# Kernel optimization log

Hardware: AMD Instinct MI355X
Metric: run time of the kernel (lower is better)

Reference implementation:

```python
import jax, jax.numpy as jnp
import numpy as np

DIM = 1024
NUM_HEADS = 16
HEAD_DIM = DIM // NUM_HEADS
ROPE_BASE = 10000.0


def _rope_cos_sin(seq_len, head_dim):
    inv_freq = 1.0 / (ROPE_BASE ** (jnp.arange(0, head_dim, 2, dtype=jnp.float32) / head_dim))
    t = jnp.arange(seq_len, dtype=jnp.float32)
    freqs = t[:, None] * inv_freq[None, :]            # [S, Dh/2]
    emb = jnp.concatenate([freqs, freqs], axis=-1)    # [S, Dh]
    return jnp.cos(emb), jnp.sin(emb)


def _rotate_half(x):
    half = x.shape[-1] // 2
    return jnp.concatenate([-x[..., half:], x[..., :half]], axis=-1)


def setup_inputs() -> dict:
    key = jax.random.key(0)
    k1, k2, k3 = jax.random.split(key, 3)
    B, S = 2, 2048
    x = jax.random.normal(k1, (B, S, DIM), dtype=jnp.float32)
    w_qkv = jax.random.normal(k2, (3 * DIM, DIM), dtype=jnp.float32) * (DIM ** -0.5)
    w_out = jax.random.normal(k3, (DIM, DIM), dtype=jnp.float32) * (DIM ** -0.5)
    return {"x": x, "w_qkv": w_qkv, "w_out": w_out}


def reference(x, w_qkv, w_out):
    B, S, D = x.shape
    H, Dh = NUM_HEADS, HEAD_DIM
    scale = Dh ** -0.5

    qkv = (x @ w_qkv.T).reshape(B, S, 3, H, Dh)      # [B,S,3,H,Dh]
    qkv = jnp.transpose(qkv, (2, 0, 3, 1, 4))        # [3,B,H,S,Dh]
    q, k, v = qkv[0], qkv[1], qkv[2]

    cos, sin = _rope_cos_sin(S, Dh)                  # [S,Dh]
    cos = cos[None, None, :, :]
    sin = sin[None, None, :, :]
    q = q * cos + _rotate_half(q) * sin
    k = k * cos + _rotate_half(k) * sin

    scores = jnp.einsum('bhqd,bhkd->bhqk', q, k) * scale
    causal_mask = jnp.triu(jnp.ones((S, S), dtype=bool), k=1)
    scores = jnp.where(causal_mask[None, None], -jnp.inf, scores)
    attn = jax.nn.softmax(scores, axis=-1)
    out = jnp.einsum('bhqk,bhkd->bhqd', attn, v)      # [B,H,S,Dh]
    out = jnp.transpose(out, (0, 2, 1, 3)).reshape(B, S, D)
    return out @ w_out.T
```

## Files before the change

### kernel.cpp

```cpp
#include <hip/hip_runtime.h>
#include <stdint.h>

typedef uint16_t u16;
typedef __attribute__((ext_vector_type(8))) short bf16x8;
typedef __attribute__((ext_vector_type(4))) float f32x4;

__device__ inline u16 f2b(float f) {
  uint32_t u = __float_as_uint(f);
  u += 0x7FFF + ((u >> 16) & 1);
  return (u16)(u >> 16);
}
__device__ inline float b2f(u16 h) {
  return __uint_as_float(((uint32_t)h) << 16);
}

typedef __attribute__((address_space(1))) void gvoid;
typedef __attribute__((address_space(3))) void lvoid;
#define GLOAD16(gp, lp)                                                        \
  __builtin_amdgcn_global_load_lds((gvoid*)(gp), (lvoid*)(lp), 16, 0, 0)

__global__ void k_detect(const u16* __restrict__ X, int* __restrict__ flag) {
  __shared__ int cnt;
  const int t = threadIdx.x;
  if (t == 0) cnt = 0;
  __syncthreads();
  float av = fabsf(b2f(X[t * 2]));
  int wild = (av < 1000.0f) ? 0 : 1;
  atomicAdd(&cnt, wild);
  __syncthreads();
  if (t == 0) flag[0] = (cnt > 16) ? 1 : 0;
}

__global__ __launch_bounds__(256, 4) void k_qkv_rope(const void* __restrict__ Xv,
                                                     const void* __restrict__ Wv,
                                                     const int* __restrict__ flag,
                                                     u16* __restrict__ Qo,
                                                     u16* __restrict__ Ko,
                                                     u16* __restrict__ Vo) {
  __shared__ u16 As[64][40];
  __shared__ u16 Bs[3][64][40];
  __shared__ float Cs[64][66];
  const int mode = flag[0];
  const int h = blockIdx.x;
  const int n0h = h * 64;
  const int m0 = blockIdx.y * 64;
  const int t = threadIdx.x, w = t >> 6, lane = t & 63;
  const int lr = lane & 15, lq = lane >> 4;
  f32x4 acc[3][4] = {};
  const int rA = t >> 2, cA = (t & 3) * 8;
  const int aoff0 = (m0 + rA) * 1024 + cA;
  const int boff0 = (n0h + rA) * 1024 + cA;

  if (mode == 0) {
    const u16* Xp = (const u16*)Xv;
    const u16* Wp = (const u16*)Wv;
    uint4 pa0 = *(const uint4*)(Xp + aoff0);
    uint4 pb0 = *(const uint4*)(Wp + boff0);
    uint4 pb1 = *(const uint4*)(Wp + boff0 + 1048576);
    uint4 pb2 = *(const uint4*)(Wp + boff0 + 2097152);
    for (int k0 = 0; k0 < 1024; k0 += 32) {
      __syncthreads();
      *(uint4*)&As[rA][cA]    = pa0;
      *(uint4*)&Bs[0][rA][cA] = pb0;
      *(uint4*)&Bs[1][rA][cA] = pb1;
      *(uint4*)&Bs[2][rA][cA] = pb2;
      __syncthreads();
      if (k0 + 32 < 1024) {
        const int kn = k0 + 32;
        pa0 = *(const uint4*)(Xp + aoff0 + kn);
        pb0 = *(const uint4*)(Wp + boff0 + kn);
        pb1 = *(const uint4*)(Wp + boff0 + 1048576 + kn);
        pb2 = *(const uint4*)(Wp + boff0 + 2097152 + kn);
      }
      bf16x8 bf[3];
#pragma unroll
      for (int e = 0; e < 3; ++e)
        bf[e] = *(const bf16x8*)&Bs[e][(w << 4) + lr][lq * 8];
#pragma unroll
      for (int mt = 0; mt < 4; ++mt) {
        bf16x8 af = *(const bf16x8*)&As[(mt << 4) + lr][lq * 8];
#pragma unroll
        for (int e = 0; e < 3; ++e)
          acc[e][mt] = __builtin_amdgcn_mfma_f32_16x16x32_bf16(af, bf[e], acc[e][mt], 0, 0, 0);
      }
    }
  } else {
    for (int k0 = 0; k0 < 1024; k0 += 32) {
      __syncthreads();
      const float* Xf = (const float*)Xv;
      const float* Wf = (const float*)Wv;
#pragma unroll
      for (int ee = 0; ee < 8; ++ee) {
        As[rA][cA + ee]    = f2b(Xf[aoff0 + k0 + ee]);
        Bs[0][rA][cA + ee] = f2b(Wf[boff0 + k0 + ee]);
        Bs[1][rA][cA + ee] = f2b(Wf[boff0 + 1048576 + k0 + ee]);
        Bs[2][rA][cA + ee] = f2b(Wf[boff0 + 2097152 + k0 + ee]);
      }
      __syncthreads();
      bf16x8 bf[3];
#pragma unroll
      for (int e = 0; e < 3; ++e)
        bf[e] = *(const bf16x8*)&Bs[e][(w << 4) + lr][lq * 8];
#pragma unroll
      for (int mt = 0; mt < 4; ++mt) {
        bf16x8 af = *(const bf16x8*)&As[(mt << 4) + lr][lq * 8];
#pragma unroll
        for (int e = 0; e < 3; ++e)
          acc[e][mt] = __builtin_amdgcn_mfma_f32_16x16x32_bf16(af, bf[e], acc[e][mt], 0, 0, 0);
      }
    }
  }

  for (int e = 0; e < 3; ++e) {
    __syncthreads();
    {
      const int col = (w << 4) + lr;
#pragma unroll
      for (int mt = 0; mt < 4; ++mt)
#pragma unroll
        for (int i = 0; i < 4; ++i)
          Cs[mt * 16 + lq * 4 + i][col] = acc[e][mt][i];
    }
    __syncthreads();
    if (e == 2) {
      const int sx = t & 63, dh0 = (t >> 6) * 16;
      const int m = m0 + sx, b = m >> 11, s = m & 2047;
      const long hb = (long)(b * 16 + h) * 64;
#pragma unroll
      for (int u = 0; u < 16; ++u) {
        int dh = dh0 + u;
        Vo[(hb + dh) * 2048 + s] = f2b(Cs[sx][dh]);
      }
    } else {
      const int r = t >> 2, dh0 = (t & 3) * 16;
      const int m = m0 + r, b = m >> 11, s = m & 2047;
      const int obase = ((b * 16 + h) * 2048 + s) * 64;
      u16* O = (e == 0) ? Qo : Ko;
#pragma unroll
      for (int u = 0; u < 16; ++u) {
        int dh = dh0 + u;
        float v  = Cs[r][dh];
        float vp = Cs[r][dh ^ 32];
        float sign = (dh < 32) ? -1.0f : 1.0f;
        float fr  = __expf((float)(dh & 31) * -0.28782314f);
        float ang = (float)s * fr;
        float sn = __sinf(ang), cs = __cosf(ang);
        O[obase + dh] = f2b(v * cs + sign * vp * sn);
      }
    }
  }
}

__device__ __forceinline__ void attn_tile(u16 QP[64][72], u16 Ks[64][72],
                                          u16 Vt[64][72], const bf16x8 qf[2],
                                          f32x4 o_acc[4], float& m_i, float& l_i,
                                          int kt, int qt_tile, int w, int lr,
                                          int lq, int lq4, int base16, int qrow_l) {
  f32x4 sa[4] = {};
#pragma unroll
  for (int mb = 0; mb < 4; ++mb)
#pragma unroll
    for (int kk = 0; kk < 2; ++kk) {
      bf16x8 kf = *(const bf16x8*)&Ks[mb * 16 + lr][kk * 32 + lq * 8];
      sa[mb] = __builtin_amdgcn_mfma_f32_16x16x32_bf16(kf, qf[kk], sa[mb], 0, 0, 0);
    }
  float sc[4][4];
  float m_new = m_i;
#pragma unroll
  for (int mb = 0; mb < 4; ++mb)
#pragma unroll
    for (int i = 0; i < 4; ++i) {
      float sv = sa[mb][i] * 0.125f;
      if (kt == qt_tile && (mb * 16 + lq4 + i) > qrow_l) sv = -3.0e4f;
      sc[mb][i] = sv;
      m_new = fmaxf(m_new, sv);
    }
  m_new = fmaxf(m_new, __shfl_xor(m_new, 16));
  m_new = fmaxf(m_new, __shfl_xor(m_new, 32));
  float alpha = __expf(m_i - m_new);
  m_i = m_new;
  float p[4][4], sm = 0.f;
#pragma unroll
  for (int mb = 0; mb < 4; ++mb)
#pragma unroll
    for (int i = 0; i < 4; ++i) { p[mb][i] = __expf(sc[mb][i] - m_new); sm += p[mb][i]; }
  sm += __shfl_xor(sm, 16);
  sm += __shfl_xor(sm, 32);
  l_i = l_i * alpha + sm;
#pragma unroll
  for (int mb = 0; mb < 4; ++mb) {
    uint2 pk;
    pk.x = (uint32_t)f2b(p[mb][0]) | ((uint32_t)f2b(p[mb][1]) << 16);
    pk.y = (uint32_t)f2b(p[mb][2]) | ((uint32_t)f2b(p[mb][3]) << 16);
    *(uint2*)&QP[w * 16 + lr][mb * 16 + lq4] = pk;
  }
#pragma unroll
  for (int i = 0; i < 4; ++i) {
    float ai = __shfl(alpha, base16 | (lq4 + i));
    o_acc[0][i] *= ai; o_acc[1][i] *= ai;
    o_acc[2][i] *= ai; o_acc[3][i] *= ai;
  }
  asm volatile("s_waitcnt lgkmcnt(0)" ::: "memory");
#pragma unroll
  for (int kk = 0; kk < 2; ++kk) {
    bf16x8 pf = *(const bf16x8*)&QP[w * 16 + lr][kk * 32 + lq * 8];
#pragma unroll
    for (int nb = 0; nb < 4; ++nb) {
      bf16x8 vf = *(const bf16x8*)&Vt[nb * 16 + lr][kk * 32 + lq * 8];
      o_acc[nb] = __builtin_amdgcn_mfma_f32_16x16x32_bf16(pf, vf, o_acc[nb], 0, 0, 0);
    }
  }
}

__global__ __launch_bounds__(256) void k_attn(const u16* __restrict__ Q,
                                              const u16* __restrict__ K,
                                              const u16* __restrict__ V,
                                              u16* __restrict__ AO) {
  __shared__ u16 QP[64][72];
  __shared__ u16 Ks[64][72];
  __shared__ u16 Vt[64][72];
  const int qtA = 31 - blockIdx.x;
  const int qtB = blockIdx.x;
  const int bh = blockIdx.y;
  const int b = bh >> 4, h = bh & 15;
  const u16* Qg = Q + (bh * 2048) * 64;
  const u16* Kg = K + bh * 2048 * 64;
  const u16* Vg = V + (long)bh * 64 * 2048;
  const int t = threadIdx.x, w = t >> 6, lane = t & 63;
  const int lr = lane & 15, lq = lane >> 4;
  const int lq4 = lq * 4;
  const int base16 = lane & 48;
  const int r0 = t >> 3, c0 = (t & 7) * 8;
  const int qrow_l = w * 16 + lr;

  bf16x8 qfA[2], qfB[2];
  *(uint4*)&QP[r0][c0]      = *(const uint4*)&Qg[(qtA * 64 + r0) * 64 + c0];
  *(uint4*)&QP[r0 + 32][c0] = *(const uint4*)&Qg[(qtA * 64 + r0 + 32) * 64 + c0];
  __syncthreads();
#pragma unroll
  for (int kk = 0; kk < 2; ++kk)
    qfA[kk] = *(const bf16x8*)&QP[w * 16 + lr][kk * 32 + lq * 8];
  __syncthreads();
  *(uint4*)&QP[r0][c0]      = *(const uint4*)&Qg[(qtB * 64 + r0) * 64 + c0];
  *(uint4*)&QP[r0 + 32][c0] = *(const uint4*)&Qg[(qtB * 64 + r0 + 32) * 64 + c0];
  __syncthreads();
#pragma unroll
  for (int kk = 0; kk < 2; ++kk)
    qfB[kk] = *(const bf16x8*)&QP[w * 16 + lr][kk * 32 + lq * 8];

  float m_iA = -3.0e4f, l_iA = 0.f, m_iB = -3.0e4f, l_iB = 0.f;
  f32x4 o_accA[4] = {}, o_accB[4] = {};

  for (int kt = 0; kt <= qtA; ++kt) {
    __syncthreads();
    *(uint4*)&Ks[r0][c0]      = *(const uint4*)&Kg[(kt * 64 + r0) * 64 + c0];
    *(uint4*)&Ks[r0 + 32][c0] = *(const uint4*)&Kg[(kt * 64 + r0 + 32) * 64 + c0];
    *(uint4*)&Vt[r0][c0]      = *(const uint4*)&Vg[r0 * 2048 + kt * 64 + c0];
    *(uint4*)&Vt[r0 + 32][c0] = *(const uint4*)&Vg[(r0 + 32) * 2048 + kt * 64 + c0];
    __syncthreads();

    attn_tile(QP, Ks, Vt, qfA, o_accA, m_iA, l_iA, kt, qtA,
              w, lr, lq, lq4, base16, qrow_l);
    if (kt <= qtB) {
      asm volatile("s_waitcnt lgkmcnt(0)" ::: "memory");
      attn_tile(QP, Ks, Vt, qfB, o_accB, m_iB, l_iB, kt, qtB,
                w, lr, lq, lq4, base16, qrow_l);
    }
  }
  float linvA = 1.0f / l_iA, linvB = 1.0f / l_iB;
#pragma unroll
  for (int i = 0; i < 4; ++i) {
    float invA = __shfl(linvA, base16 | (lq4 + i));
    float invB = __shfl(linvB, base16 | (lq4 + i));
    int rowA = qtA * 64 + w * 16 + lq4 + i;
    int rowB = qtB * 64 + w * 16 + lq4 + i;
    int obA = (b * 2048 + rowA) * 1024 + h * 64;
    int obB = (b * 2048 + rowB) * 1024 + h * 64;
#pragma unroll
    for (int nb = 0; nb < 4; ++nb) {
      AO[obA + nb * 16 + lr] = f2b(o_accA[nb][i] * invA);
      AO[obB + nb * 16 + lr] = f2b(o_accB[nb][i] * invB);
    }
  }
}

__global__ __launch_bounds__(256) void k_gemm_out(const u16* __restrict__ A,
                                                  const void* __restrict__ Bv,
                                                  const int* __restrict__ flag,
                                                  void* __restrict__ Cv) {
  __shared__ u16 As[2][64][32];
  __shared__ u16 Bs[2][2][64][32];
  const int mode = flag[0];
  const int n0 = blockIdx.x * 128, m0 = blockIdx.y * 64;
  const int t = threadIdx.x, w = t >> 6, lane = t & 63;
  const int lr = lane & 15, lq = lane >> 4;
  f32x4 acc[2][4] = {};
  const int rA = t >> 2;
  const int gcol = (((t & 3) ^ ((rA >> 1) & 3)) << 3);
  const int aoff  = (m0 + rA) * 1024 + gcol;
  const int boff0 = (n0 + rA) * 1024 + gcol;
  const int boff1 = boff0 + 65536;

  if (mode == 0) {
    const u16* Bp = (const u16*)Bv;
#define STAGE_OUT(buf, kk)                                                     \
    do {                                                                       \
      GLOAD16(A + aoff + (kk),   &As[buf][(w << 4)][0]);                       \
      GLOAD16(Bp + boff0 + (kk), &Bs[buf][0][(w << 4)][0]);                    \
      GLOAD16(Bp + boff1 + (kk), &Bs[buf][1][(w << 4)][0]);                    \
    } while (0)
    STAGE_OUT(0, 0);
    asm volatile("s_waitcnt vmcnt(0)" ::: "memory");
    __syncthreads();
    int cur = 0;
    for (int k0 = 0; k0 < 1024; k0 += 32) {
      if (k0 + 32 < 1024) STAGE_OUT(cur ^ 1, k0 + 32);
      bf16x8 bfx[2];
      const int rowB = (w << 4) + lr;
      const int scB = ((lq ^ ((rowB >> 1) & 3)) << 3);
#pragma unroll
      for (int e = 0; e < 2; ++e)
        bfx[e] = *(const bf16x8*)&Bs[cur][e][rowB][scB];
#pragma unroll
      for (int mt = 0; mt < 4; ++mt) {
        const int row = (mt << 4) + lr;
        const int sc = ((lq ^ ((row >> 1) & 3)) << 3);
        bf16x8 af = *(const bf16x8*)&As[cur][row][sc];
#pragma unroll
        for (int e = 0; e < 2; ++e)
          acc[e][mt] = __builtin_amdgcn_mfma_f32_16x16x32_bf16(af, bfx[e], acc[e][mt], 0, 0, 0);
      }
      __syncthreads();
      cur ^= 1;
    }
#undef STAGE_OUT
  } else {
    const float* Bf = (const float*)Bv;
    for (int k0 = 0; k0 < 1024; k0 += 32) {
      __syncthreads();
      *(uint4*)&As[0][rA][(t & 3) << 3] = *(const uint4*)(A + (m0 + rA) * 1024 + ((t & 3) << 3) + k0);
#pragma unroll
      for (int ee = 0; ee < 8; ++ee) {
        const int pc = ((t & 3) << 3) + ee;
        Bs[0][0][rA][pc] = f2b(Bf[(n0 + rA) * 1024 + pc + k0]);
        Bs[0][1][rA][pc] = f2b(Bf[(n0 + rA) * 1024 + 65536 + pc + k0]);
      }
      __syncthreads();
      bf16x8 bfx[2];
      const int rowB = (w << 4) + lr;
#pragma unroll
      for (int e = 0; e < 2; ++e)
        bfx[e] = *(const bf16x8*)&Bs[0][e][rowB][lq * 8];
#pragma unroll
      for (int mt = 0; mt < 4; ++mt) {
        bf16x8 af = *(const bf16x8*)&As[0][(mt << 4) + lr][lq * 8];
#pragma unroll
        for (int e = 0; e < 2; ++e)
          acc[e][mt] = __builtin_amdgcn_mfma_f32_16x16x32_bf16(af, bfx[e], acc[e][mt], 0, 0, 0);
      }
    }
  }
#pragma unroll
  for (int e = 0; e < 2; ++e) {
    const int col = n0 + e * 64 + (w << 4) + lr;
    if (mode == 0) {
      u16* C = (u16*)Cv;
#pragma unroll
      for (int mt = 0; mt < 4; ++mt)
#pragma unroll
        for (int i = 0; i < 4; ++i)
          C[(m0 + mt * 16 + lq * 4 + i) * 1024 + col] = f2b(acc[e][mt][i]);
    } else {
      float* C = (float*)Cv;
#pragma unroll
      for (int mt = 0; mt < 4; ++mt)
#pragma unroll
        for (int i = 0; i < 4; ++i)
          C[(m0 + mt * 16 + lq * 4 + i) * 1024 + col] = acc[e][mt][i];
    }
  }
}

extern "C" void kernel_launch(void* const* d_in, const int* in_sizes, int n_in,
                              void* d_out, int out_size, void* d_ws, size_t ws_size,
                              hipStream_t stream) {
  const void* x    = d_in[0];
  const void* wqkv = d_in[1];
  const void* wout = d_in[2];

  int* flag = (int*)d_ws;
  u16* qb = (u16*)((char*)d_ws + 256);
  u16* kb = qb + 4194304;
  u16* vb = kb + 4194304;
  u16* ao = vb + 4194304;

  k_detect  <<<dim3(1), 256, 0, stream>>>((const u16*)x, flag);
  k_qkv_rope<<<dim3(16, 64), 256, 0, stream>>>(x, wqkv, flag, qb, kb, vb);
  k_attn    <<<dim3(16, 32), 256, 0, stream>>>(qb, kb, vb, ao);
  k_gemm_out<<<dim3(8, 64), 256, 0, stream>>>(ao, wout, flag, d_out);
}
```

Measured before the change: 245.6 us.

## Inline dtype probe, double QKV row tile, prefetch K/V tiles in attention

Removes the separate detection kernel by having each GEMM block probe the input dtype itself, which saves one launch and one dependency. The QKV+RoPE kernel now computes 128 rows per block instead of 64, so each weight tile loaded is reused twice, at the cost of more accumulators and fewer blocks. The attention kernel now loads the next K/V tile into registers while the current one is being computed. The out-projection probes W_out rather than x, and that probe is an extra per-block read.

Result: faster. 219.5 us (-10.6%).

```diff
diff --git a/kernel.cpp b/kernel.cpp
--- a/kernel.cpp
+++ b/kernel.cpp
@@ -19,48 +19,49 @@
 #define GLOAD16(gp, lp)                                                        \
   __builtin_amdgcn_global_load_lds((gvoid*)(gp), (lvoid*)(lp), 16, 0, 0)
 
-__global__ void k_detect(const u16* __restrict__ X, int* __restrict__ flag) {
-  __shared__ int cnt;
-  const int t = threadIdx.x;
-  if (t == 0) cnt = 0;
+__device__ __forceinline__ int probe_mode(const u16* __restrict__ P, int t,
+                                          int* cnt_sh) {
+  if (t == 0) *cnt_sh = 0;
   __syncthreads();
-  float av = fabsf(b2f(X[t * 2]));
-  int wild = (av < 1000.0f) ? 0 : 1;
-  atomicAdd(&cnt, wild);
+  float av = fabsf(b2f(P[t * 2]));
+  if (av >= 1000.0f) atomicAdd(cnt_sh, 1);
   __syncthreads();
-  if (t == 0) flag[0] = (cnt > 16) ? 1 : 0;
-}
-
-__global__ __launch_bounds__(256, 4) void k_qkv_rope(const void* __restrict__ Xv,
-                                                     const void* __restrict__ Wv,
-                                                     const int* __restrict__ flag,
-                                                     u16* __restrict__ Qo,
-                                                     u16* __restrict__ Ko,
-                                                     u16* __restrict__ Vo) {
-  __shared__ u16 As[64][40];
+  return (*cnt_sh > 16) ? 1 : 0;
+}
+
+__global__ __launch_bounds__(256) void k_qkv_rope(const void* __restrict__ Xv,
+                                                  const void* __restrict__ Wv,
+                                                  u16* __restrict__ Qo,
+                                                  u16* __restrict__ Ko,
+                                                  u16* __restrict__ Vo) {
+  __shared__ u16 As[2][64][40];
   __shared__ u16 Bs[3][64][40];
   __shared__ float Cs[64][66];
-  const int mode = flag[0];
+  __shared__ int cnt_sh;
+  const int t = threadIdx.x, w = t >> 6, lane = t & 63;
+  const int mode = probe_mode((const u16*)Xv, t, &cnt_sh);
   const int h = blockIdx.x;
   const int n0h = h * 64;
-  const int m0 = blockIdx.y * 64;
-  const int t = threadIdx.x, w = t >> 6, lane = t & 63;
+  const int m0 = blockIdx.y * 128;
   const int lr = lane & 15, lq = lane >> 4;
-  f32x4 acc[3][4] = {};
+  f32x4 acc[3][2][4] = {};
   const int rA = t >> 2, cA = (t & 3) * 8;
   const int aoff0 = (m0 + rA) * 1024 + cA;
+  const int aoff1 = (m0 + 64 + rA) * 1024 + cA;
   const int boff0 = (n0h + rA) * 1024 + cA;
 
   if (mode == 0) {
     const u16* Xp = (const u16*)Xv;
     const u16* Wp = (const u16*)Wv;
     uint4 pa0 = *(const uint4*)(Xp + aoff0);
+    uint4 pa1 = *(const uint4*)(Xp + aoff1);
     uint4 pb0 = *(const uint4*)(Wp + boff0);
     uint4 pb1 = *(const uint4*)(Wp + boff0 + 1048576);
     uint4 pb2 = *(const uint4*)(Wp + boff0 + 2097152);
     for (int k0 = 0; k0 < 1024; k0 += 32) {
       __syncthreads();
-      *(uint4*)&As[rA][cA]    = pa0;
+      *(uint4*)&As[0][rA][cA] = pa0;
+      *(uint4*)&As[1][rA][cA] = pa1;
       *(uint4*)&Bs[0][rA][cA] = pb0;
       *(uint4*)&Bs[1][rA][cA] = pb1;
       *(uint4*)&Bs[2][rA][cA] = pb2;
@@ -68,6 +69,7 @@
       if (k0 + 32 < 1024) {
         const int kn = k0 + 32;
         pa0 = *(const uint4*)(Xp + aoff0 + kn);
+        pa1 = *(const uint4*)(Xp + aoff1 + kn);
         pb0 = *(const uint4*)(Wp + boff0 + kn);
         pb1 = *(const uint4*)(Wp + boff0 + 1048576 + kn);
         pb2 = *(const uint4*)(Wp + boff0 + 2097152 + kn);
@@ -78,10 +80,13 @@
         bf[e] = *(const bf16x8*)&Bs[e][(w << 4) + lr][lq * 8];
 #pragma unroll
       for (int mt = 0; mt < 4; ++mt) {
-        bf16x8 af = *(const bf16x8*)&As[(mt << 4) + lr][lq * 8];
-#pragma unroll
-        for (int e = 0; e < 3; ++e)
-          acc[e][mt] = __builtin_amdgcn_mfma_f32_16x16x32_bf16(af, bf[e], acc[e][mt], 0, 0, 0);
+        bf16x8 af0 = *(const bf16x8*)&As[0][(mt << 4) + lr][lq * 8];
+        bf16x8 af1 = *(const bf16x8*)&As[1][(mt << 4) + lr][lq * 8];
+#pragma unroll
+        for (int e = 0; e < 3; ++e) {
+          acc[e][0][mt] = __builtin_amdgcn_mfma_f32_16x16x32_bf16(af0, bf[e], acc[e][0][mt], 0, 0, 0);
+          acc[e][1][mt] = __builtin_amdgcn_mfma_f32_16x16x32_bf16(af1, bf[e], acc[e][1][mt], 0, 0, 0);
+        }
       }
     }
   } else {
@@ -91,7 +96,8 @@
       const float* Wf = (const float*)Wv;
 #pragma unroll
       for (int ee = 0; ee < 8; ++ee) {
-        As[rA][cA + ee]    = f2b(Xf[aoff0 + k0 + ee]);
+        As[0][rA][cA + ee] = f2b(Xf[aoff0 + k0 + ee]);
+        As[1][rA][cA + ee] = f2b(Xf[aoff1 + k0 + ee]);
         Bs[0][rA][cA + ee] = f2b(Wf[boff0 + k0 + ee]);
         Bs[1][rA][cA + ee] = f2b(Wf[boff0 + 1048576 + k0 + ee]);
         Bs[2][rA][cA + ee] = f2b(Wf[boff0 + 2097152 + k0 + ee]);
@@ -103,49 +109,55 @@
         bf[e] = *(const bf16x8*)&Bs[e][(w << 4) + lr][lq * 8];
 #pragma unroll
       for (int mt = 0; mt < 4; ++mt) {
-        bf16x8 af = *(const bf16x8*)&As[(mt << 4) + lr][lq * 8];
-#pragma unroll
-        for (int e = 0; e < 3; ++e)
-          acc[e][mt] = __builtin_amdgcn_mfma_f32_16x16x32_bf16(af, bf[e], acc[e][mt], 0, 0, 0);
-      }
-    }
-  }
-
-  for (int e = 0; e < 3; ++e) {
-    __syncthreads();
-    {
-      const int col = (w << 4) + lr;
-#pragma unroll
-      for (int mt = 0; mt < 4; ++mt)
-#pragma unroll
-        for (int i = 0; i < 4; ++i)
-          Cs[mt * 16 + lq * 4 + i][col] = acc[e][mt][i];
-    }
-    __syncthreads();
-    if (e == 2) {
-      const int sx = t & 63, dh0 = (t >> 6) * 16;
-      const int m = m0 + sx, b = m >> 11, s = m & 2047;
-      const long hb = (long)(b * 16 + h) * 64;
-#pragma unroll
-      for (int u = 0; u < 16; ++u) {
-        int dh = dh0 + u;
-        Vo[(hb + dh) * 2048 + s] = f2b(Cs[sx][dh]);
-      }
-    } else {
-      const int r = t >> 2, dh0 = (t & 3) * 16;
-      const int m = m0 + r, b = m >> 11, s = m & 2047;
-      const int obase = ((b * 16 + h) * 2048 + s) * 64;
-      u16* O = (e == 0) ? Qo : Ko;
-#pragma unroll
-      for (int u = 0; u < 16; ++u) {
-        int dh = dh0 + u;
-        float v  = Cs[r][dh];
-        float vp = Cs[r][dh ^ 32];
-        float sign = (dh < 32) ? -1.0f : 1.0f;
-        float fr  = __expf((float)(dh & 31) * -0.28782314f);
-        float ang = (float)s * fr;
-        float sn = __sinf(ang), cs = __cosf(ang);
-        O[obase + dh] = f2b(v * cs + sign * vp * sn);
+        bf16x8 af0 = *(const bf16x8*)&As[0][(mt << 4) + lr][lq * 8];
+        bf16x8 af1 = *(const bf16x8*)&As[1][(mt << 4) + lr][lq * 8];
+#pragma unroll
+        for (int e = 0; e < 3; ++e) {
+          acc[e][0][mt] = __builtin_amdgcn_mfma_f32_16x16x32_bf16(af0, bf[e], acc[e][0][mt], 0, 0, 0);
+          acc[e][1][mt] = __builtin_amdgcn_mfma_f32_16x16x32_bf16(af1, bf[e], acc[e][1][mt], 0, 0, 0);
+        }
+      }
+    }
+  }
+
+  for (int f = 0; f < 2; ++f) {
+    const int m0f = m0 + f * 64;
+    for (int e = 0; e < 3; ++e) {
+      __syncthreads();
+      {
+        const int col = (w << 4) + lr;
+#pragma unroll
+        for (int mt = 0; mt < 4; ++mt)
+#pragma unroll
+          for (int i = 0; i < 4; ++i)
+            Cs[mt * 16 + lq * 4 + i][col] = acc[e][f][mt][i];
+      }
+      __syncthreads();
+      if (e == 2) {
+        const int sx = t & 63, dh0 = (t >> 6) * 16;
+        const int m = m0f + sx, b = m >> 11, s = m & 2047;
+        const long hb = (long)(b * 16 + h) * 64;
+#pragma unroll
+        for (int u = 0; u < 16; ++u) {
+          int dh = dh0 + u;
+          Vo[(hb + dh) * 2048 + s] = f2b(Cs[sx][dh]);
+        }
+      } else {
+        const int r = t >> 2, dh0 = (t & 3) * 16;
+        const int m = m0f + r, b = m >> 11, s = m & 2047;
+        const int obase = ((b * 16 + h) * 2048 + s) * 64;
+        u16* O = (e == 0) ? Qo : Ko;
+#pragma unroll
+        for (int u = 0; u < 16; ++u) {
+          int dh = dh0 + u;
+          float v  = Cs[r][dh];
+          float vp = Cs[r][dh ^ 32];
+          float sign = (dh < 32) ? -1.0f : 1.0f;
+          float fr  = __expf((float)(dh & 31) * -0.28782314f);
+          float ang = (float)s * fr;
+          float sn = __sinf(ang), cs = __cosf(ang);
+          O[obase + dh] = f2b(v * cs + sign * vp * sn);
+        }
       }
     }
   }
@@ -233,6 +245,11 @@
   const int r0 = t >> 3, c0 = (t & 7) * 8;
   const int qrow_l = w * 16 + lr;
 
+  uint4 pk0 = *(const uint4*)&Kg[r0 * 64 + c0];
+  uint4 pk1 = *(const uint4*)&Kg[(r0 + 32) * 64 + c0];
+  uint4 pv0 = *(const uint4*)&Vg[r0 * 2048 + c0];
+  uint4 pv1 = *(const uint4*)&Vg[(r0 + 32) * 2048 + c0];
+
   bf16x8 qfA[2], qfB[2];
   *(uint4*)&QP[r0][c0]      = *(const uint4*)&Qg[(qtA * 64 + r0) * 64 + c0];
   *(uint4*)&QP[r0 + 32][c0] = *(const uint4*)&Qg[(qtA * 64 + r0 + 32) * 64 + c0];
@@ -253,11 +270,18 @@
 
   for (int kt = 0; kt <= qtA; ++kt) {
     __syncthreads();
-    *(uint4*)&Ks[r0][c0]      = *(const uint4*)&Kg[(kt * 64 + r0) * 64 + c0];
-    *(uint4*)&Ks[r0 + 32][c0] = *(const uint4*)&Kg[(kt * 64 + r0 + 32) * 64 + c0];
-    *(uint4*)&Vt[r0][c0]      = *(const uint4*)&Vg[r0 * 2048 + kt * 64 + c0];
-    *(uint4*)&Vt[r0 + 32][c0] = *(const uint4*)&Vg[(r0 + 32) * 2048 + kt * 64 + c0];
+    *(uint4*)&Ks[r0][c0]      = pk0;
+    *(uint4*)&Ks[r0 + 32][c0] = pk1;
+    *(uint4*)&Vt[r0][c0]      = pv0;
+    *(uint4*)&Vt[r0 + 32][c0] = pv1;
     __syncthreads();
+    if (kt < qtA) {
+      const int kn = kt + 1;
+      pk0 = *(const uint4*)&Kg[(kn * 64 + r0) * 64 + c0];
+      pk1 = *(const uint4*)&Kg[(kn * 64 + r0 + 32) * 64 + c0];
+      pv0 = *(const uint4*)&Vg[r0 * 2048 + kn * 64 + c0];
+      pv1 = *(const uint4*)&Vg[(r0 + 32) * 2048 + kn * 64 + c0];
+    }
 
     attn_tile(QP, Ks, Vt, qfA, o_accA, m_iA, l_iA, kt, qtA,
               w, lr, lq, lq4, base16, qrow_l);
@@ -286,13 +310,13 @@
 
 __global__ __launch_bounds__(256) void k_gemm_out(const u16* __restrict__ A,
                                                   const void* __restrict__ Bv,
-                                                  const int* __restrict__ flag,
                                                   void* __restrict__ Cv) {
   __shared__ u16 As[2][64][32];
   __shared__ u16 Bs[2][2][64][32];
-  const int mode = flag[0];
+  __shared__ int cnt_sh;
+  const int t = threadIdx.x, w = t >> 6, lane = t & 63;
+  const int mode = probe_mode((const u16*)Bv, t, &cnt_sh);
   const int n0 = blockIdx.x * 128, m0 = blockIdx.y * 64;
-  const int t = threadIdx.x, w = t >> 6, lane = t & 63;
   const int lr = lane & 15, lq = lane >> 4;
   f32x4 acc[2][4] = {};
   const int rA = t >> 2;
@@ -388,14 +412,12 @@
   const void* wqkv = d_in[1];
   const void* wout = d_in[2];
 
-  int* flag = (int*)d_ws;
   u16* qb = (u16*)((char*)d_ws + 256);
   u16* kb = qb + 4194304;
   u16* vb = kb + 4194304;
   u16* ao = vb + 4194304;
 
-  k_detect  <<<dim3(1), 256, 0, stream>>>((const u16*)x, flag);
-  k_qkv_rope<<<dim3(16, 64), 256, 0, stream>>>(x, wqkv, flag, qb, kb, vb);
+  k_qkv_rope<<<dim3(16, 32), 256, 0, stream>>>(x, wqkv, qb, kb, vb);
   k_attn    <<<dim3(16, 32), 256, 0, stream>>>(qb, kb, vb, ao);
-  k_gemm_out<<<dim3(8, 64), 256, 0, stream>>>(ao, wout, flag, d_out);
-}
+  k_gemm_out<<<dim3(8, 64), 256, 0, stream>>>(ao, wout, d_out);
+}
```
